# Performance work log

Hardware: AMD Instinct MI355X
Metric: run time of the kernel (lower is better)

Reference implementation:

```python
import jax, jax.numpy as jnp
import numpy as np

TAU = 0.1
HARD_K = 32
MIN_OVERLAP = 4
PAIR_WEIGHTS = [("view", "cart", 0.2), ("cart", "purchase", 1.0), ("view", "purchase", 1.0)]


def setup_inputs() -> dict:
    key = jax.random.key(0)
    ks = jax.random.split(key, 6)
    U, D = 100000, 128
    return {
        "emb_view": jax.random.normal(ks[0], (U, D), dtype=jnp.float32),
        "emb_cart": jax.random.normal(ks[1], (U, D), dtype=jnp.float32),
        "emb_purchase": jax.random.normal(ks[2], (U, D), dtype=jnp.float32),
        "users_view": jax.random.randint(ks[3], (20000,), 0, U, dtype=jnp.int64),
        "users_cart": jax.random.randint(ks[4], (15000,), 0, U, dtype=jnp.int64),
        "users_purchase": jax.random.randint(ks[5], (10000,), 0, U, dtype=jnp.int64),
    }


def _l2norm(x):
    # F.normalize(x, dim=-1): x / max(||x||, eps)
    n = jnp.linalg.norm(x, axis=-1, keepdims=True)
    return x / jnp.maximum(n, 1e-12)


def _directional(z_weak, z_strong, tau, hard_k):
    N = z_strong.shape[0]
    if N < 2:
        return jnp.zeros((), dtype=z_strong.dtype)
    z_w = _l2norm(jax.lax.stop_gradient(z_weak))  # weak side is detached
    z_s = _l2norm(z_strong)
    sim = (z_s @ z_w.T) / tau  # [N, N]
    pos = jnp.diagonal(sim)    # positive logits, labels = arange(N)
    n_hard = min(hard_k, N - 1)
    if 0 < n_hard < N - 1:
        neg_only = jnp.where(jnp.eye(N, dtype=bool), -jnp.inf, sim)
        hard_neg, _ = jax.lax.top_k(neg_only, n_hard)          # [N, n_hard]
        logits = jnp.concatenate([pos[:, None], hard_neg], 1)  # [N, 1+n_hard]
        return jnp.mean(jax.scipy.special.logsumexp(logits, axis=1) - pos)
    # full-softmax CE with label i for row i
    return jnp.mean(jax.scipy.special.logsumexp(sim, axis=1) - pos)


def reference(emb_view, emb_cart, emb_purchase, users_view, users_cart, users_purchase):
    embs = {"view": emb_view, "cart": emb_cart, "purchase": emb_purchase}
    users = {
        "view": np.asarray(users_view),
        "cart": np.asarray(users_cart),
        "purchase": np.asarray(users_purchase),
    }
    loss = jnp.zeros((), dtype=emb_view.dtype)
    for weak, strong, w in PAIR_WEIGHTS:
        u_w, u_s = users[weak], users[strong]
        if u_w.size == 0 or u_s.size == 0:
            continue
        # common_pair = u_w[isin(u_w, u_s)] : keeps u_w order and duplicates
        common = u_w[np.isin(u_w, u_s)]
        if common.size < MIN_OVERLAP:
            continue
        idx = jnp.asarray(common)
        loss = loss + w * _directional(embs[weak][idx], embs[strong][idx], TAU, HARD_K)
    return loss
```

## Files before the change

kernel.cpp:

```cpp
#include <hip/hip_runtime.h>
#include <hip/hip_bf16.h>
#include <math.h>

#define D 128
#define NEG_INF (-3.0e38f)
#define LDA 136

#define C0 3200
#define C1 1792
#define C2 2304
#define T0 25
#define T1 14
#define T2 18

typedef __attribute__((ext_vector_type(8))) short bf16x8;
typedef __attribute__((ext_vector_type(8))) unsigned short u16x8;
typedef __attribute__((ext_vector_type(4))) float f32x4;

__device__ __forceinline__ float wredf_add(float v) {
#pragma unroll
  for (int m = 32; m; m >>= 1) v += __shfl_xor(v, m, 64);
  return v;
}
__device__ __forceinline__ float wredf_max(float v) {
#pragma unroll
  for (int m = 32; m; m >>= 1) v = fmaxf(v, __shfl_xor(v, m, 64));
  return v;
}
__device__ __forceinline__ float wredf_min(float v) {
#pragma unroll
  for (int m = 32; m; m >>= 1) v = fminf(v, __shfl_xor(v, m, 64));
  return v;
}
__device__ __forceinline__ int wredi_add(int v) {
#pragma unroll
  for (int m = 32; m; m >>= 1) v += __shfl_xor(v, m, 64);
  return v;
}

__global__ void build_masks_k(const int* __restrict__ uc, int nc,
                              const int* __restrict__ up, int npu,
                              unsigned* __restrict__ mc, unsigned* __restrict__ mp) {
  int t = blockIdx.x * blockDim.x + threadIdx.x;
  if (t < nc) {
    int u = uc[t];
    atomicOr(&mc[u >> 5], 1u << (u & 31));
  } else {
    int t2 = t - nc;
    if (t2 < npu) {
      int u = up[t2];
      atomicOr(&mp[u >> 5], 1u << (u & 31));
    }
  }
}

__global__ void filter_k(const int* __restrict__ uv, int nv,
                         const int* __restrict__ uc, int nc,
                         const unsigned* __restrict__ mc, const unsigned* __restrict__ mp,
                         int* __restrict__ c0, int* __restrict__ c1, int* __restrict__ c2,
                         int* __restrict__ counts, int s1, int s2) {
  int t = blockIdx.x * blockDim.x + threadIdx.x;
  int lane = threadIdx.x & 63;
  const int* src;
  const unsigned* m;
  int* dst;
  int* cnt;
  int n, cap, base;
  if (t < s1) {
    src = uv; n = nv; m = mc; dst = c0; cnt = counts + 0; cap = C0; base = t;
  } else if (t < s2) {
    src = uc; n = nc; m = mp; dst = c1; cnt = counts + 1; cap = C1; base = t - s1;
  } else {
    src = uv; n = nv; m = mp; dst = c2; cnt = counts + 2; cap = C2; base = t - s2;
  }
  bool match = false;
  int u = 0;
  if (base < n) {
    u = src[base];
    match = (m[u >> 5] >> (u & 31)) & 1u;
  }
  unsigned long long b = __ballot(match);
  int tot = __popcll(b);
  int idx0 = 0;
  if (lane == 0 && tot) idx0 = atomicAdd(cnt, tot);
  idx0 = __shfl(idx0, 0, 64);
  if (match) {
    int p = idx0 + __popcll(b & ((1ull << lane) - 1));
    if (p < cap) dst[p] = u;
  }
}

struct GatherArgs {
  const float* emb[6];
  const int* com[6];
  const int* cnt[6];
  short* dst[6];
  int start[7];
};

__global__ __launch_bounds__(256) void gather_norm_k(GatherArgs ga) {
  int wid = threadIdx.x >> 6, lane = threadIdx.x & 63;
  int g = blockIdx.x * 4 + wid;
  if (g >= ga.start[6]) return;
  int s = 0;
#pragma unroll
  for (int t = 1; t < 6; ++t)
    if (g >= ga.start[t]) s = t;
  int r = g - ga.start[s];
  int cap = ga.start[s + 1] - ga.start[s];
  int N = min(*ga.cnt[s], cap);
  short* drow = ga.dst[s] + (size_t)r * D + lane * 2;
  if (r >= N) {
    *(ushort2*)drow = make_ushort2(0, 0);
    return;
  }
  int u = ga.com[s][r];
  const float* src = ga.emb[s] + (size_t)u * D;
  float2 v = *(const float2*)(src + lane * 2);
  float ss = v.x * v.x + v.y * v.y;
  ss = wredf_add(ss);
  float inv = 1.0f / fmaxf(sqrtf(ss), 1e-12f);
  __hip_bfloat16 h0 = __float2bfloat16(v.x * inv);
  __hip_bfloat16 h1 = __float2bfloat16(v.y * inv);
  ushort2 o;
  o.x = *(unsigned short*)&h0;
  o.y = *(unsigned short*)&h1;
  *(ushort2*)drow = o;
}

__device__ __forceinline__ void gemm_tile(const short* __restrict__ A, const short* __restrict__ B,
                                          unsigned short* __restrict__ C, int ldc, int bx, int by,
                                          short* As, short* Bs, int tid) {
  int rb = by * 128, cb = bx * 128;
  int rrow = tid >> 4, rcol = (tid & 15) * 8;
#pragma unroll
  for (int pass = 0; pass < 8; ++pass) {
    int row = pass * 16 + rrow;
    uint4 va = *(const uint4*)(A + (size_t)(rb + row) * D + rcol);
    uint4 vb = *(const uint4*)(B + (size_t)(cb + row) * D + rcol);
    *(uint4*)(&As[row * LDA + rcol]) = va;
    *(uint4*)(&Bs[row * LDA + rcol]) = vb;
  }
  __syncthreads();
  int wave = tid >> 6, lane = tid & 63;
  int wr = (wave >> 1) * 64, wc = (wave & 1) * 64;
  int ln = lane & 15, quad = lane >> 4;
  f32x4 acc[4][4] = {};
#pragma unroll
  for (int ks = 0; ks < 4; ++ks) {
    int ko = ks * 32 + quad * 8;
    bf16x8 af[4], bg[4];
#pragma unroll
    for (int i = 0; i < 4; ++i) af[i] = *(const bf16x8*)(&As[(wr + i * 16 + ln) * LDA + ko]);
#pragma unroll
    for (int j = 0; j < 4; ++j) bg[j] = *(const bf16x8*)(&Bs[(wc + j * 16 + ln) * LDA + ko]);
#pragma unroll
    for (int i = 0; i < 4; ++i)
#pragma unroll
      for (int j = 0; j < 4; ++j)
        acc[i][j] = __builtin_amdgcn_mfma_f32_16x16x32_bf16(af[i], bg[j], acc[i][j], 0, 0, 0);
  }
#pragma unroll
  for (int i = 0; i < 4; ++i)
#pragma unroll
    for (int j = 0; j < 4; ++j) {
      int col = cb + wc + j * 16 + ln;
#pragma unroll
      for (int r = 0; r < 4; ++r) {
        int row = rb + wr + i * 16 + quad * 4 + r;
        __hip_bfloat16 h = __float2bfloat16(acc[i][j][r] * 10.0f);
        C[(size_t)row * ldc + col] = *(unsigned short*)&h;
      }
    }
}

struct GemmAllArgs {
  const short *zs0, *zw0, *zs1, *zw1, *zs2, *zw2;
  unsigned short *s0, *s1, *s2;
};

__global__ __launch_bounds__(256) void gemm_all_k(GemmAllArgs ga) {
  __shared__ __align__(16) short As[128 * LDA];
  __shared__ __align__(16) short Bs[128 * LDA];
  int tid = threadIdx.x;
  int b = blockIdx.x;
  if (b < T0 * T0) {
    gemm_tile(ga.zs0, ga.zw0, ga.s0, C0, b % T0, b / T0, As, Bs, tid);
  } else if (b < T0 * T0 + T1 * T1) {
    int t = b - T0 * T0;
    gemm_tile(ga.zs1, ga.zw1, ga.s1, C1, t % T1, t / T1, As, Bs, tid);
  } else {
    int t = b - T0 * T0 - T1 * T1;
    gemm_tile(ga.zs2, ga.zw2, ga.s2, C2, t % T2, t / T2, As, Bs, tid);
  }
}

template <int NL>
__device__ __forceinline__ void select_rows(const unsigned short* __restrict__ sim, int ldc, int N,
                                            int i, int lane, double* __restrict__ slot) {
  const unsigned short* row = sim + (size_t)i * ldc;
  float vals[NL * 8];
  float posl = NEG_INF;
#pragma unroll
  for (int L = 0; L < NL; ++L) {
    int base = L * 512 + lane * 8;
    u16x8 raw = {0, 0, 0, 0, 0, 0, 0, 0};
    if (L * 512 < N) raw = *(const u16x8*)(row + base);
#pragma unroll
    for (int c = 0; c < 8; ++c) {
      int j = base + c;
      float v = __uint_as_float((unsigned)raw[c] << 16);
      if (j >= N) v = NEG_INF;
      if (j == i) { posl = v; v = NEG_INF; }
      vals[L * 8 + c] = v;
    }
  }
  float pos = __shfl(posl, (i & 511) >> 3, 64);
  float m = NEG_INF;
#pragma unroll
  for (int s = 0; s < NL * 8; ++s) m = fmaxf(m, vals[s]);
  m = wredf_max(m);
  int K = min(32, N - 1);
  float lo = -20.0f, hi = m + 1e-3f;
  for (int it = 0; it < 16; ++it) {
    float mid = 0.5f * (lo + hi);
    int c = 0;
#pragma unroll
    for (int s = 0; s < NL * 8; ++s) c += (vals[s] > mid) ? 1 : 0;
    c = wredi_add(c);
    if (c >= K) lo = mid; else hi = mid;
  }
  float M = fmaxf(m, pos);
  float sum = 0.0f, vmin = 3.0e38f;
  int cnt = 0;
#pragma unroll
  for (int s = 0; s < NL * 8; ++s) {
    float v = vals[s];
    bool in = v > lo;
    float e = __expf(v - M);
    if (in) { sum += e; cnt++; vmin = fminf(vmin, v); }
  }
  sum = wredf_add(sum);
  cnt = wredi_add(cnt);
  vmin = wredf_min(vmin);
  float corr = (cnt > K) ? (float)(cnt - K) * __expf(vmin - M) : 0.0f;
  float lse = M + __logf(sum - corr + __expf(pos - M));
  if (lane == 0) atomicAdd(slot, (double)(lse - pos));
}

__global__ __launch_bounds__(256) void select_all_k(const unsigned short* __restrict__ sim0,
                                                    const unsigned short* __restrict__ sim1,
                                                    const unsigned short* __restrict__ sim2,
                                                    const int* __restrict__ counts,
                                                    double* __restrict__ partials) {
  int wid = threadIdx.x >> 6, lane = threadIdx.x & 63;
  int b = blockIdx.x;
  if (b < C0 / 4) {
    int N = min(counts[0], C0);
    int i = b * 4 + wid;
    if (i < N) select_rows<7>(sim0, C0, N, i, lane, partials + 0 * 64 + (b & 63));
  } else if (b < C0 / 4 + C1 / 4) {
    int bb = b - C0 / 4;
    int N = min(counts[1], C1);
    int i = bb * 4 + wid;
    if (i < N) select_rows<4>(sim1, C1, N, i, lane, partials + 64 + (bb & 63));
  } else {
    int bb = b - C0 / 4 - C1 / 4;
    int N = min(counts[2], C2);
    int i = bb * 4 + wid;
    if (i < N) select_rows<5>(sim2, C2, N, i, lane, partials + 128 + (bb & 63));
  }
}

__global__ void finalize_k(const int* __restrict__ counts, const double* __restrict__ partials,
                           float* __restrict__ out, int ok) {
  if (threadIdx.x != 0 || blockIdx.x != 0) return;
  if (!ok) { out[0] = -12345.0f; return; }
  const float w[3] = {0.2f, 1.0f, 1.0f};
  const int caps[3] = {C0, C1, C2};
  float tot = 0.0f;
  for (int p = 0; p < 3; ++p) {
    double s = 0.0;
    for (int k = 0; k < 64; ++k) s += partials[p * 64 + k];
    int N = min(counts[p], caps[p]);
    if (N >= 4) tot += w[p] * (float)(s / (double)N);
  }
  out[0] = tot;
}

extern "C" void kernel_launch(void* const* d_in, const int* in_sizes, int n_in,
                              void* d_out, int out_size, void* d_ws, size_t ws_size,
                              hipStream_t stream) {
  const float* emb_view = (const float*)d_in[0];
  const float* emb_cart = (const float*)d_in[1];
  const float* emb_pur  = (const float*)d_in[2];
  const int* u_view = (const int*)d_in[3];
  const int* u_cart = (const int*)d_in[4];
  const int* u_pur  = (const int*)d_in[5];
  int nv = in_sizes[3], nc = in_sizes[4], np = in_sizes[5];
  int U = in_sizes[0] / D;

  size_t off = 2048;
  auto alloc = [&](size_t b) {
    size_t o = (off + 255) & ~(size_t)255;
    off = o + b;
    return o;
  };
  size_t maskWords = (size_t)(U + 31) / 32;
  size_t mask0_off = alloc(maskWords * 4);
  size_t mask1_off = alloc(maskWords * 4);
  size_t zero_end = off;
  size_t com0_off = alloc((size_t)C0 * 4);
  size_t com1_off = alloc((size_t)C1 * 4);
  size_t com2_off = alloc((size_t)C2 * 4);
  size_t zw0_off = alloc((size_t)C0 * D * 2);
  size_t zs0_off = alloc((size_t)C0 * D * 2);
  size_t zw1_off = alloc((size_t)C1 * D * 2);
  size_t zs1_off = alloc((size_t)C1 * D * 2);
  size_t zw2_off = alloc((size_t)C2 * D * 2);
  size_t zs2_off = alloc((size_t)C2 * D * 2);
  size_t sim0_off = alloc((size_t)C0 * C0 * 2);
  size_t sim1_off = alloc((size_t)C1 * C1 * 2);
  size_t sim2_off = alloc((size_t)C2 * C2 * 2);
  (void)alloc(1024);
  int ws_ok = (off <= ws_size) ? 1 : 0;

  char* ws = (char*)d_ws;
  int* counts = (int*)ws;
  double* partials = (double*)(ws + 256);
  unsigned* mask_c = (unsigned*)(ws + mask0_off);
  unsigned* mask_p = (unsigned*)(ws + mask1_off);
  int* com0 = (int*)(ws + com0_off);
  int* com1 = (int*)(ws + com1_off);
  int* com2 = (int*)(ws + com2_off);
  short* zw0 = (short*)(ws + zw0_off);
  short* zs0 = (short*)(ws + zs0_off);
  short* zw1 = (short*)(ws + zw1_off);
  short* zs1 = (short*)(ws + zs1_off);
  short* zw2 = (short*)(ws + zw2_off);
  short* zs2 = (short*)(ws + zs2_off);
  unsigned short* sim0 = (unsigned short*)(ws + sim0_off);
  unsigned short* sim1 = (unsigned short*)(ws + sim1_off);
  unsigned short* sim2 = (unsigned short*)(ws + sim2_off);

  if (ws_ok) {
    hipMemsetAsync(d_ws, 0, zero_end, stream);

    int t_masks = nc + np;
    build_masks_k<<<(t_masks + 255) / 256, 256, 0, stream>>>(u_cart, nc, u_pur, np, mask_c, mask_p);

    int s1 = ((nv + 255) / 256) * 256;
    int s2 = s1 + ((nc + 255) / 256) * 256;
    int t_filt = s2 + ((nv + 255) / 256) * 256;
    filter_k<<<t_filt / 256, 256, 0, stream>>>(u_view, nv, u_cart, nc, mask_c, mask_p,
                                               com0, com1, com2, counts, s1, s2);

    GatherArgs ga;
    const float* embs[6] = {emb_view, emb_cart, emb_cart, emb_pur, emb_view, emb_pur};
    const int* coms[6] = {com0, com0, com1, com1, com2, com2};
    const int* cnts[6] = {counts + 0, counts + 0, counts + 1, counts + 1, counts + 2, counts + 2};
    short* dsts[6] = {zw0, zs0, zw1, zs1, zw2, zs2};
    int caps6[6] = {C0, C0, C1, C1, C2, C2};
    int cum = 0;
    for (int s = 0; s < 6; ++s) {
      ga.emb[s] = embs[s];
      ga.com[s] = coms[s];
      ga.cnt[s] = cnts[s];
      ga.dst[s] = dsts[s];
      ga.start[s] = cum;
      cum += caps6[s];
    }
    ga.start[6] = cum;
    gather_norm_k<<<cum / 4, 256, 0, stream>>>(ga);

    GemmAllArgs gar;
    gar.zs0 = zs0; gar.zw0 = zw0; gar.s0 = sim0;
    gar.zs1 = zs1; gar.zw1 = zw1; gar.s1 = sim1;
    gar.zs2 = zs2; gar.zw2 = zw2; gar.s2 = sim2;
    gemm_all_k<<<T0 * T0 + T1 * T1 + T2 * T2, 256, 0, stream>>>(gar);

    select_all_k<<<C0 / 4 + C1 / 4 + C2 / 4, 256, 0, stream>>>(sim0, sim1, sim2, counts, partials);
  }

  finalize_k<<<1, 1, 0, stream>>>(counts, partials, (float*)d_out, ws_ok);
}
```

Before: 217.0 us.

## Fuse filter with gather-normalize, skip empty GEMM tiles, fold finalize into select

Merges filtering and embedding gather/normalization into one kernel in which each wave normalizes its matched rows directly, removing the common-index buffers and one launch. GEMM tiles beyond the actual overlap count are skipped, and outputs are staged through shared memory for coalesced 16-byte stores. Finalize moves into the select kernel through a last-block atomic counter. Bisection counting uses ballot/popcount instead of shuffle reductions, with a tighter lower bound. This trades more zeroing in the memset (the z buffers now need zero padding) and serial per-wave gathers for fewer launches and less wasted GEMM work.

```diff
diff --git a/kernel.cpp b/kernel.cpp
--- a/kernel.cpp
+++ b/kernel.cpp
@@ -12,6 +12,8 @@
 #define T0 25
 #define T1 14
 #define T2 18
+#define NTILES (T0 * T0 + T1 * T1 + T2 * T2)
+#define NSEL (C0 / 4 + C1 / 4 + C2 / 4)
 
 typedef __attribute__((ext_vector_type(8))) short bf16x8;
 typedef __attribute__((ext_vector_type(8))) unsigned short u16x8;
@@ -32,15 +34,15 @@
   for (int m = 32; m; m >>= 1) v = fminf(v, __shfl_xor(v, m, 64));
   return v;
 }
-__device__ __forceinline__ int wredi_add(int v) {
+__device__ __forceinline__ double wredd_add(double v) {
 #pragma unroll
   for (int m = 32; m; m >>= 1) v += __shfl_xor(v, m, 64);
   return v;
 }
 
-__global__ void build_masks_k(const int* __restrict__ uc, int nc,
-                              const int* __restrict__ up, int npu,
-                              unsigned* __restrict__ mc, unsigned* __restrict__ mp) {
+__global__ void masks_k(const int* __restrict__ uc, int nc,
+                        const int* __restrict__ up, int npu,
+                        unsigned* __restrict__ mc, unsigned* __restrict__ mp) {
   int t = blockIdx.x * blockDim.x + threadIdx.x;
   if (t < nc) {
     int u = uc[t];
@@ -54,84 +56,76 @@
   }
 }
 
-__global__ void filter_k(const int* __restrict__ uv, int nv,
-                         const int* __restrict__ uc, int nc,
-                         const unsigned* __restrict__ mc, const unsigned* __restrict__ mp,
-                         int* __restrict__ c0, int* __restrict__ c1, int* __restrict__ c2,
-                         int* __restrict__ counts, int s1, int s2) {
-  int t = blockIdx.x * blockDim.x + threadIdx.x;
+struct FGArgs {
+  const int* src[3];
+  int n[3];
+  const unsigned* mask[3];
+  const float* embW[3];
+  const float* embS[3];
+  short* zw[3];
+  short* zs[3];
+  int cap[3];
+  int seg1, seg2;
+  int* counts;
+};
+
+__global__ __launch_bounds__(256) void filtgather_k(FGArgs a) {
+  int t = blockIdx.x * 256 + threadIdx.x;
   int lane = threadIdx.x & 63;
-  const int* src;
-  const unsigned* m;
-  int* dst;
-  int* cnt;
-  int n, cap, base;
-  if (t < s1) {
-    src = uv; n = nv; m = mc; dst = c0; cnt = counts + 0; cap = C0; base = t;
-  } else if (t < s2) {
-    src = uc; n = nc; m = mp; dst = c1; cnt = counts + 1; cap = C1; base = t - s1;
-  } else {
-    src = uv; n = nv; m = mp; dst = c2; cnt = counts + 2; cap = C2; base = t - s2;
-  }
+  int s, base;
+  if (t < a.seg1) { s = 0; base = t; }
+  else if (t < a.seg2) { s = 1; base = t - a.seg1; }
+  else { s = 2; base = t - a.seg2; }
   bool match = false;
   int u = 0;
-  if (base < n) {
-    u = src[base];
-    match = (m[u >> 5] >> (u & 31)) & 1u;
+  if (base < a.n[s]) {
+    u = a.src[s][base];
+    match = (a.mask[s][u >> 5] >> (u & 31)) & 1u;
   }
   unsigned long long b = __ballot(match);
   int tot = __popcll(b);
+  if (!tot) return;
   int idx0 = 0;
-  if (lane == 0 && tot) idx0 = atomicAdd(cnt, tot);
+  if (lane == 0) idx0 = atomicAdd(a.counts + s, tot);
   idx0 = __shfl(idx0, 0, 64);
-  if (match) {
-    int p = idx0 + __popcll(b & ((1ull << lane) - 1));
-    if (p < cap) dst[p] = u;
-  }
-}
-
-struct GatherArgs {
-  const float* emb[6];
-  const int* com[6];
-  const int* cnt[6];
-  short* dst[6];
-  int start[7];
+  const float* eW = a.embW[s];
+  const float* eS = a.embS[s];
+  short* zw = a.zw[s];
+  short* zs = a.zs[s];
+  int cap = a.cap[s];
+  unsigned long long bb = b;
+  for (int k = 0; k < tot; ++k) {
+    int sl = __builtin_ctzll(bb);
+    bb &= bb - 1;
+    int p = idx0 + k;
+    if (p >= cap) break;
+    int uu = __shfl(u, sl, 64);
+    float2 vw = *(const float2*)(eW + (size_t)uu * D + lane * 2);
+    float2 vs = *(const float2*)(eS + (size_t)uu * D + lane * 2);
+    float ssw = wredf_add(vw.x * vw.x + vw.y * vw.y);
+    float sss = wredf_add(vs.x * vs.x + vs.y * vs.y);
+    float iw = 1.0f / fmaxf(sqrtf(ssw), 1e-12f);
+    float is = 1.0f / fmaxf(sqrtf(sss), 1e-12f);
+    __hip_bfloat16 w0 = __float2bfloat16(vw.x * iw), w1 = __float2bfloat16(vw.y * iw);
+    __hip_bfloat16 s0 = __float2bfloat16(vs.x * is), s1 = __float2bfloat16(vs.y * is);
+    *(ushort2*)(zw + (size_t)p * D + lane * 2) =
+        make_ushort2(*(unsigned short*)&w0, *(unsigned short*)&w1);
+    *(ushort2*)(zs + (size_t)p * D + lane * 2) =
+        make_ushort2(*(unsigned short*)&s0, *(unsigned short*)&s1);
+  }
+}
+
+struct GemmArgs {
+  const short *zs0, *zw0, *zs1, *zw1, *zs2, *zw2;
+  unsigned short *s0, *s1, *s2;
+  const int* counts;
 };
-
-__global__ __launch_bounds__(256) void gather_norm_k(GatherArgs ga) {
-  int wid = threadIdx.x >> 6, lane = threadIdx.x & 63;
-  int g = blockIdx.x * 4 + wid;
-  if (g >= ga.start[6]) return;
-  int s = 0;
-#pragma unroll
-  for (int t = 1; t < 6; ++t)
-    if (g >= ga.start[t]) s = t;
-  int r = g - ga.start[s];
-  int cap = ga.start[s + 1] - ga.start[s];
-  int N = min(*ga.cnt[s], cap);
-  short* drow = ga.dst[s] + (size_t)r * D + lane * 2;
-  if (r >= N) {
-    *(ushort2*)drow = make_ushort2(0, 0);
-    return;
-  }
-  int u = ga.com[s][r];
-  const float* src = ga.emb[s] + (size_t)u * D;
-  float2 v = *(const float2*)(src + lane * 2);
-  float ss = v.x * v.x + v.y * v.y;
-  ss = wredf_add(ss);
-  float inv = 1.0f / fmaxf(sqrtf(ss), 1e-12f);
-  __hip_bfloat16 h0 = __float2bfloat16(v.x * inv);
-  __hip_bfloat16 h1 = __float2bfloat16(v.y * inv);
-  ushort2 o;
-  o.x = *(unsigned short*)&h0;
-  o.y = *(unsigned short*)&h1;
-  *(ushort2*)drow = o;
-}
 
 __device__ __forceinline__ void gemm_tile(const short* __restrict__ A, const short* __restrict__ B,
                                           unsigned short* __restrict__ C, int ldc, int bx, int by,
-                                          short* As, short* Bs, int tid) {
+                                          int N, short* As, short* Bs, int tid) {
   int rb = by * 128, cb = bx * 128;
+  if (rb >= N || cb >= N) return;
   int rrow = tid >> 4, rcol = (tid & 15) * 8;
 #pragma unroll
   for (int pass = 0; pass < 8; ++pass) {
@@ -160,38 +154,45 @@
       for (int j = 0; j < 4; ++j)
         acc[i][j] = __builtin_amdgcn_mfma_f32_16x16x32_bf16(af[i], bg[j], acc[i][j], 0, 0, 0);
   }
+  __syncthreads();
 #pragma unroll
   for (int i = 0; i < 4; ++i)
 #pragma unroll
     for (int j = 0; j < 4; ++j) {
-      int col = cb + wc + j * 16 + ln;
+      int tcol = wc + j * 16 + ln;
 #pragma unroll
       for (int r = 0; r < 4; ++r) {
-        int row = rb + wr + i * 16 + quad * 4 + r;
+        int trow = wr + i * 16 + quad * 4 + r;
         __hip_bfloat16 h = __float2bfloat16(acc[i][j][r] * 10.0f);
-        C[(size_t)row * ldc + col] = *(unsigned short*)&h;
+        As[trow * LDA + tcol] = *(short*)&h;
       }
     }
-}
-
-struct GemmAllArgs {
-  const short *zs0, *zw0, *zs1, *zw1, *zs2, *zw2;
-  unsigned short *s0, *s1, *s2;
-};
-
-__global__ __launch_bounds__(256) void gemm_all_k(GemmAllArgs ga) {
+  __syncthreads();
+#pragma unroll
+  for (int pass = 0; pass < 8; ++pass) {
+    int idx = pass * 256 + tid;
+    int row = idx >> 4, c8 = (idx & 15) * 8;
+    *(uint4*)(C + (size_t)(rb + row) * ldc + cb + c8) = *(const uint4*)(&As[row * LDA + c8]);
+  }
+  __syncthreads();
+}
+
+__global__ __launch_bounds__(256) void gemm_all_k(GemmArgs g) {
   __shared__ __align__(16) short As[128 * LDA];
   __shared__ __align__(16) short Bs[128 * LDA];
   int tid = threadIdx.x;
   int b = blockIdx.x;
   if (b < T0 * T0) {
-    gemm_tile(ga.zs0, ga.zw0, ga.s0, C0, b % T0, b / T0, As, Bs, tid);
+    int N = min(g.counts[0], C0);
+    gemm_tile(g.zs0, g.zw0, g.s0, C0, b % T0, b / T0, N, As, Bs, tid);
   } else if (b < T0 * T0 + T1 * T1) {
     int t = b - T0 * T0;
-    gemm_tile(ga.zs1, ga.zw1, ga.s1, C1, t % T1, t / T1, As, Bs, tid);
+    int N = min(g.counts[1], C1);
+    gemm_tile(g.zs1, g.zw1, g.s1, C1, t % T1, t / T1, N, As, Bs, tid);
   } else {
     int t = b - T0 * T0 - T1 * T1;
-    gemm_tile(ga.zs2, ga.zw2, ga.s2, C2, t % T2, t / T2, As, Bs, tid);
+    int N = min(g.counts[2], C2);
+    gemm_tile(g.zs2, g.zw2, g.s2, C2, t % T2, t / T2, N, As, Bs, tid);
   }
 }
 
@@ -221,13 +222,12 @@
   for (int s = 0; s < NL * 8; ++s) m = fmaxf(m, vals[s]);
   m = wredf_max(m);
   int K = min(32, N - 1);
-  float lo = -20.0f, hi = m + 1e-3f;
+  float lo = -10.2f, hi = m + 1e-3f;
   for (int it = 0; it < 16; ++it) {
     float mid = 0.5f * (lo + hi);
     int c = 0;
 #pragma unroll
-    for (int s = 0; s < NL * 8; ++s) c += (vals[s] > mid) ? 1 : 0;
-    c = wredi_add(c);
+    for (int s = 0; s < NL * 8; ++s) c += __popcll(__ballot(vals[s] > mid));
     if (c >= K) lo = mid; else hi = mid;
   }
   float M = fmaxf(m, pos);
@@ -237,22 +237,26 @@
   for (int s = 0; s < NL * 8; ++s) {
     float v = vals[s];
     bool in = v > lo;
-    float e = __expf(v - M);
-    if (in) { sum += e; cnt++; vmin = fminf(vmin, v); }
+    cnt += __popcll(__ballot(in));
+    if (in) {
+      sum += __expf(v - M);
+      vmin = fminf(vmin, v);
+    }
   }
   sum = wredf_add(sum);
-  cnt = wredi_add(cnt);
   vmin = wredf_min(vmin);
   float corr = (cnt > K) ? (float)(cnt - K) * __expf(vmin - M) : 0.0f;
   float lse = M + __logf(sum - corr + __expf(pos - M));
   if (lane == 0) atomicAdd(slot, (double)(lse - pos));
 }
 
-__global__ __launch_bounds__(256) void select_all_k(const unsigned short* __restrict__ sim0,
+__global__ __launch_bounds__(256) void select_fin_k(const unsigned short* __restrict__ sim0,
                                                     const unsigned short* __restrict__ sim1,
                                                     const unsigned short* __restrict__ sim2,
                                                     const int* __restrict__ counts,
-                                                    double* __restrict__ partials) {
+                                                    double* __restrict__ partials,
+                                                    unsigned* __restrict__ done,
+                                                    float* __restrict__ out) {
   int wid = threadIdx.x >> 6, lane = threadIdx.x & 63;
   int b = blockIdx.x;
   if (b < C0 / 4) {
@@ -270,22 +274,35 @@
     int i = bb * 4 + wid;
     if (i < N) select_rows<5>(sim2, C2, N, i, lane, partials + 128 + (bb & 63));
   }
-}
-
-__global__ void finalize_k(const int* __restrict__ counts, const double* __restrict__ partials,
-                           float* __restrict__ out, int ok) {
-  if (threadIdx.x != 0 || blockIdx.x != 0) return;
-  if (!ok) { out[0] = -12345.0f; return; }
-  const float w[3] = {0.2f, 1.0f, 1.0f};
-  const int caps[3] = {C0, C1, C2};
-  float tot = 0.0f;
-  for (int p = 0; p < 3; ++p) {
-    double s = 0.0;
-    for (int k = 0; k < 64; ++k) s += partials[p * 64 + k];
-    int N = min(counts[p], caps[p]);
-    if (N >= 4) tot += w[p] * (float)(s / (double)N);
-  }
-  out[0] = tot;
+  __shared__ int lastf;
+  __shared__ double ps[4];
+  __syncthreads();
+  if (threadIdx.x == 0) {
+    __threadfence();
+    unsigned old = atomicAdd(done, 1u);
+    lastf = (old == (unsigned)(gridDim.x - 1)) ? 1 : 0;
+  }
+  __syncthreads();
+  if (!lastf) return;
+  double v = 0.0;
+  if (threadIdx.x < 192) v = atomicAdd(&partials[threadIdx.x], 0.0);
+  v = wredd_add(v);
+  if (lane == 0 && wid < 3) ps[wid] = v;
+  __syncthreads();
+  if (threadIdx.x == 0) {
+    const float w[3] = {0.2f, 1.0f, 1.0f};
+    const int caps[3] = {C0, C1, C2};
+    float tot = 0.0f;
+    for (int p = 0; p < 3; ++p) {
+      int N = min(counts[p], caps[p]);
+      if (N >= 4) tot += w[p] * (float)(ps[p] / (double)N);
+    }
+    out[0] = tot;
+  }
+}
+
+__global__ void sentinel_k(float* out) {
+  if (threadIdx.x == 0 && blockIdx.x == 0) out[0] = -12345.0f;
 }
 
 extern "C" void kernel_launch(void* const* d_in, const int* in_sizes, int n_in,
@@ -300,25 +317,23 @@
   int nv = in_sizes[3], nc = in_sizes[4], np = in_sizes[5];
   int U = in_sizes[0] / D;
 
-  size_t off = 2048;
+  size_t off = 64;
   auto alloc = [&](size_t b) {
     size_t o = (off + 255) & ~(size_t)255;
     off = o + b;
     return o;
   };
-  size_t maskWords = (size_t)(U + 31) / 32;
-  size_t mask0_off = alloc(maskWords * 4);
-  size_t mask1_off = alloc(maskWords * 4);
-  size_t zero_end = off;
-  size_t com0_off = alloc((size_t)C0 * 4);
-  size_t com1_off = alloc((size_t)C1 * 4);
-  size_t com2_off = alloc((size_t)C2 * 4);
+  size_t partials_off = alloc(192 * 8);
+  size_t maskBytes = ((size_t)(U + 31) / 32) * 4;
+  size_t mask0_off = alloc(maskBytes);
+  size_t mask1_off = alloc(maskBytes);
   size_t zw0_off = alloc((size_t)C0 * D * 2);
   size_t zs0_off = alloc((size_t)C0 * D * 2);
   size_t zw1_off = alloc((size_t)C1 * D * 2);
   size_t zs1_off = alloc((size_t)C1 * D * 2);
   size_t zw2_off = alloc((size_t)C2 * D * 2);
   size_t zs2_off = alloc((size_t)C2 * D * 2);
+  size_t zero_end = off;
   size_t sim0_off = alloc((size_t)C0 * C0 * 2);
   size_t sim1_off = alloc((size_t)C1 * C1 * 2);
   size_t sim2_off = alloc((size_t)C2 * C2 * 2);
@@ -326,13 +341,16 @@
   int ws_ok = (off <= ws_size) ? 1 : 0;
 
   char* ws = (char*)d_ws;
+  if (!ws_ok) {
+    sentinel_k<<<1, 1, 0, stream>>>((float*)d_out);
+    return;
+  }
+
   int* counts = (int*)ws;
-  double* partials = (double*)(ws + 256);
+  unsigned* done = (unsigned*)(ws + 12);
+  double* partials = (double*)(ws + partials_off);
   unsigned* mask_c = (unsigned*)(ws + mask0_off);
   unsigned* mask_p = (unsigned*)(ws + mask1_off);
-  int* com0 = (int*)(ws + com0_off);
-  int* com1 = (int*)(ws + com1_off);
-  int* com2 = (int*)(ws + com2_off);
   short* zw0 = (short*)(ws + zw0_off);
   short* zs0 = (short*)(ws + zs0_off);
   short* zw1 = (short*)(ws + zw1_off);
@@ -343,44 +361,30 @@
   unsigned short* sim1 = (unsigned short*)(ws + sim1_off);
   unsigned short* sim2 = (unsigned short*)(ws + sim2_off);
 
-  if (ws_ok) {
-    hipMemsetAsync(d_ws, 0, zero_end, stream);
-
-    int t_masks = nc + np;
-    build_masks_k<<<(t_masks + 255) / 256, 256, 0, stream>>>(u_cart, nc, u_pur, np, mask_c, mask_p);
-
-    int s1 = ((nv + 255) / 256) * 256;
-    int s2 = s1 + ((nc + 255) / 256) * 256;
-    int t_filt = s2 + ((nv + 255) / 256) * 256;
-    filter_k<<<t_filt / 256, 256, 0, stream>>>(u_view, nv, u_cart, nc, mask_c, mask_p,
-                                               com0, com1, com2, counts, s1, s2);
-
-    GatherArgs ga;
-    const float* embs[6] = {emb_view, emb_cart, emb_cart, emb_pur, emb_view, emb_pur};
-    const int* coms[6] = {com0, com0, com1, com1, com2, com2};
-    const int* cnts[6] = {counts + 0, counts + 0, counts + 1, counts + 1, counts + 2, counts + 2};
-    short* dsts[6] = {zw0, zs0, zw1, zs1, zw2, zs2};
-    int caps6[6] = {C0, C0, C1, C1, C2, C2};
-    int cum = 0;
-    for (int s = 0; s < 6; ++s) {
-      ga.emb[s] = embs[s];
-      ga.com[s] = coms[s];
-      ga.cnt[s] = cnts[s];
-      ga.dst[s] = dsts[s];
-      ga.start[s] = cum;
-      cum += caps6[s];
-    }
-    ga.start[6] = cum;
-    gather_norm_k<<<cum / 4, 256, 0, stream>>>(ga);
-
-    GemmAllArgs gar;
-    gar.zs0 = zs0; gar.zw0 = zw0; gar.s0 = sim0;
-    gar.zs1 = zs1; gar.zw1 = zw1; gar.s1 = sim1;
-    gar.zs2 = zs2; gar.zw2 = zw2; gar.s2 = sim2;
-    gemm_all_k<<<T0 * T0 + T1 * T1 + T2 * T2, 256, 0, stream>>>(gar);
-
-    select_all_k<<<C0 / 4 + C1 / 4 + C2 / 4, 256, 0, stream>>>(sim0, sim1, sim2, counts, partials);
-  }
-
-  finalize_k<<<1, 1, 0, stream>>>(counts, partials, (float*)d_out, ws_ok);
-}
+  hipMemsetAsync(d_ws, 0, zero_end, stream);
+
+  masks_k<<<(nc + np + 255) / 256, 256, 0, stream>>>(u_cart, nc, u_pur, np, mask_c, mask_p);
+
+  FGArgs fa;
+  fa.src[0] = u_view; fa.n[0] = nv; fa.mask[0] = mask_c;
+  fa.embW[0] = emb_view; fa.embS[0] = emb_cart; fa.zw[0] = zw0; fa.zs[0] = zs0; fa.cap[0] = C0;
+  fa.src[1] = u_cart; fa.n[1] = nc; fa.mask[1] = mask_p;
+  fa.embW[1] = emb_cart; fa.embS[1] = emb_pur; fa.zw[1] = zw1; fa.zs[1] = zs1; fa.cap[1] = C1;
+  fa.src[2] = u_view; fa.n[2] = nv; fa.mask[2] = mask_p;
+  fa.embW[2] = emb_view; fa.embS[2] = emb_pur; fa.zw[2] = zw2; fa.zs[2] = zs2; fa.cap[2] = C2;
+  fa.seg1 = ((nv + 255) / 256) * 256;
+  fa.seg2 = fa.seg1 + ((nc + 255) / 256) * 256;
+  int t_filt = fa.seg2 + ((nv + 255) / 256) * 256;
+  fa.counts = counts;
+  filtgather_k<<<t_filt / 256, 256, 0, stream>>>(fa);
+
+  GemmArgs g;
+  g.zs0 = zs0; g.zw0 = zw0; g.s0 = sim0;
+  g.zs1 = zs1; g.zw1 = zw1; g.s1 = sim1;
+  g.zs2 = zs2; g.zw2 = zw2; g.s2 = sim2;
+  g.counts = counts;
+  gemm_all_k<<<NTILES, 256, 0, stream>>>(g);
+
+  select_fin_k<<<NSEL, 256, 0, stream>>>(sim0, sim1, sim2, counts, partials, done,
+                                         (float*)d_out);
+}
```

Result: slower. 236.9 us (+9.2%).
